# Performance work log

Measured on AMD Instinct MI355X. Metric: run time of the kernel, lower is better.

The kernel has to match this reference:

```python
import jax, jax.numpy as jnp
import numpy as np

HIDDEN = 4096
N_HEADS = 32
N_KV = 8
HEAD_DIM = HIDDEN // N_HEADS  # 128
ROT_DIM = int(HEAD_DIM * 0.5)  # partial_rotary_factor = 0.5 -> 64
ROPE_BASE = 1_000_000.0
EPS = 1e-6
T = 2048


def setup_inputs() -> dict:
    key = jax.random.key(0)
    k1, k2, k3, k4, k5 = jax.random.split(key, 5)
    qkv_out = (N_HEADS + 2 * N_KV) * HEAD_DIM  # 6144
    hidden_states = jax.random.normal(k1, (T, HIDDEN), dtype=jnp.float32)
    positions = jnp.arange(T, dtype=jnp.int32)
    w_qkv = jax.random.normal(k2, (HIDDEN, qkv_out), dtype=jnp.float32) * (HIDDEN ** -0.5)
    w_o = jax.random.normal(k3, (N_HEADS * HEAD_DIM, HIDDEN), dtype=jnp.float32) * ((N_HEADS * HEAD_DIM) ** -0.5)
    q_norm_w = jnp.ones((HEAD_DIM,), dtype=jnp.float32) + 0.01 * jax.random.normal(k4, (HEAD_DIM,), dtype=jnp.float32)
    k_norm_w = jnp.ones((HEAD_DIM,), dtype=jnp.float32) + 0.01 * jax.random.normal(k5, (HEAD_DIM,), dtype=jnp.float32)
    return {"hidden_states": hidden_states, "positions": positions,
            "w_qkv": w_qkv, "w_o": w_o, "q_norm_w": q_norm_w, "k_norm_w": k_norm_w}


def _rms_norm(x, w):
    # x: [T, H, D]; normalize over last dim
    var = jnp.mean(jnp.square(x), axis=-1, keepdims=True)
    return x * jax.lax.rsqrt(var + EPS) * w


def _apply_rope(x, positions):
    # neox-style rotary on first ROT_DIM dims of head_dim; rest passes through
    half = ROT_DIM // 2
    inv_freq = 1.0 / (ROPE_BASE ** (jnp.arange(0, ROT_DIM, 2, dtype=jnp.float32) / ROT_DIM))
    freqs = positions.astype(jnp.float32)[:, None] * inv_freq[None, :]  # [T, half]
    cos = jnp.cos(freqs)[:, None, :]  # [T, 1, half]
    sin = jnp.sin(freqs)[:, None, :]
    x_rot, x_pass = x[..., :ROT_DIM], x[..., ROT_DIM:]
    x1, x2 = x_rot[..., :half], x_rot[..., half:]
    rot = jnp.concatenate([x1 * cos - x2 * sin, x2 * cos + x1 * sin], axis=-1)
    return jnp.concatenate([rot, x_pass], axis=-1)


def reference(hidden_states, positions, w_qkv, w_o, q_norm_w, k_norm_w):
    q_size = N_HEADS * HEAD_DIM
    kv_size = N_KV * HEAD_DIM
    qkv = hidden_states @ w_qkv  # [T, q+2kv]
    q = qkv[:, :q_size].reshape(-1, N_HEADS, HEAD_DIM)
    k = qkv[:, q_size:q_size + kv_size].reshape(-1, N_KV, HEAD_DIM)
    v = qkv[:, q_size + kv_size:].reshape(-1, N_KV, HEAD_DIM)
    q = _rms_norm(q, q_norm_w)
    k = _rms_norm(k, k_norm_w)
    q = _apply_rope(q, positions)
    k = _apply_rope(k, positions)
    # GQA: repeat kv heads
    rep = N_HEADS // N_KV
    k = jnp.repeat(k, rep, axis=1)  # [T, H, D]
    v = jnp.repeat(v, rep, axis=1)
    scale = HEAD_DIM ** -0.5
    scores = jnp.einsum('thd,shd->hts', q, k) * scale  # [H, T, T]
    t = hidden_states.shape[0]
    causal = jnp.tril(jnp.ones((t, t), dtype=bool))
    scores = jnp.where(causal[None], scores, jnp.float32(-1e30))
    probs = jax.nn.softmax(scores, axis=-1)
    o = jnp.einsum('hts,shd->thd', probs, v).reshape(t, N_HEADS * HEAD_DIM)
    return o @ w_o
```

## Files before the change

kernel.cpp:

```cpp
#include <hip/hip_runtime.h>
#include <math.h>

#define HIDDEN 4096
#define QKV_N 6144
#define T_LEN 2048
#define HD 128
#define N_HEADS 32
#define N_KV 8
#define SCALE 0.08838834764831845f

typedef unsigned short u16;
typedef unsigned int u32;
typedef __attribute__((ext_vector_type(8))) short bf16x8;
typedef __attribute__((ext_vector_type(4))) float f32x4;

__device__ __forceinline__ u16 f2b(float x) {
  u32 u = __builtin_bit_cast(u32, x);
  u += 0x7fffu + ((u >> 16) & 1u);
  return (u16)(u >> 16);
}

typedef const __attribute__((address_space(1))) void* gas_ptr;
typedef __attribute__((address_space(3))) void* las_ptr;
__device__ __forceinline__ void gll16(const void* g, void* l) {
  __builtin_amdgcn_global_load_lds((gas_ptr)g, (las_ptr)l, 16, 0, 0);
}

__global__ __launch_bounds__(256) void cast_bf16_kernel(
    const float* __restrict__ in, u16* __restrict__ out) {
  const size_t i = ((size_t)blockIdx.x * 256 + threadIdx.x) * 4;
  f32x4 v = *(const f32x4*)(in + i);
  ushort4 o;
  o.x = f2b(v[0]); o.y = f2b(v[1]); o.z = f2b(v[2]); o.w = f2b(v[3]);
  *(ushort4*)(out + i) = o;
}

__global__ __launch_bounds__(256) void transpose_cast_kernel(
    const float* __restrict__ W, u16* __restrict__ WT, int K, int N) {
  __shared__ float t[32][33];
  const int n0 = blockIdx.x * 32, k0 = blockIdx.y * 32;
  const int c = threadIdx.x & 31;
  const int r0 = threadIdx.x >> 5;
#pragma unroll
  for (int j = 0; j < 4; ++j) {
    const int r = r0 + 8 * j;
    t[c][r] = W[(size_t)(k0 + r) * N + n0 + c];
  }
  __syncthreads();
#pragma unroll
  for (int j = 0; j < 4; ++j) {
    const int n = r0 + 8 * j;
    WT[(size_t)(n0 + n) * K + k0 + c] = f2b(t[n][c]);
  }
}

template <int BM, int BN, bool ROPE>
__global__ __launch_bounds__(512, 2) void gemm256_kernel(
    const u16* __restrict__ A, const u16* __restrict__ BT,
    float* __restrict__ C, int M, int N, int K,
    const int* __restrict__ positions, float2* __restrict__ ropeTab) {
  if constexpr (ROPE) {
    if (blockIdx.y == gridDim.y - 1) {
      for (int i = blockIdx.x * 512 + threadIdx.x; i < T_LEN * 32;
           i += gridDim.x * 512) {
        const int t = i >> 5, idx = i & 31;
        const float invf = powf(1.0e6f, -(float)idx * (1.0f / 32.0f));
        const float fr = (float)positions[t] * invf;
        ropeTab[i] = make_float2(cosf(fr), sinf(fr));
      }
      return;
    }
  }
  constexpr int WCOLS = BN / 4;
  constexpr int NF = WCOLS / 16;
  constexpr int NF2 = NF / 2;
  constexpr int MF = BM / 32;
  constexpr int ALOADS = BM / 128;
  constexpr int BLOADS = BN / 128;
  constexpr int VMN = ALOADS + BLOADS;
  __shared__ __align__(16) u16 As[2][2][BM * 32];
  __shared__ __align__(16) u16 Bs[2][2][BN * 32];

  const int tid = threadIdx.x;
  const int w = tid >> 6, l = tid & 63;
  const int wr = w >> 2, wc = w & 3;
  const int m = l & 15, g = l >> 4;
  const int bm = blockIdx.y * BM, bn = blockIdx.x * BN;
  const int NT = K >> 6;

  size_t gA[2]; int sA[2];
  size_t gB[2]; int sB[2];
#pragma unroll
  for (int i = 0; i < ALOADS; ++i) {
    const int s = i * 512 + tid;
    const int r = s >> 2, o = s & 3;
    sA[i] = s * 8;
    gA[i] = (size_t)(bm + r) * K + (o ^ ((r >> 1) & 3)) * 8;
  }
#pragma unroll
  for (int i = 0; i < BLOADS; ++i) {
    const int s = i * 512 + tid;
    const int r = s >> 2, o = s & 3;
    sB[i] = s * 8;
    gB[i] = (size_t)(bn + r) * K + (o ^ ((r >> 1) & 3)) * 8;
  }

  const int foff = m * 32 + ((g ^ ((m >> 1) & 3)) * 8);
  const int abase = wr * (BM / 2) * 32;
  const int bbase = wc * WCOLS * 32;

#define STAGE_A(tile, kh)                                                      \
  {                                                                            \
    const size_t kofs = (size_t)(tile) * 64 + (kh) * 32;                       \
    u16* dst = &As[(tile) & 1][kh][0];                                         \
    gll16(A + gA[0] + kofs, dst + sA[0]);                                      \
    if constexpr (ALOADS > 1) gll16(A + gA[1] + kofs, dst + sA[1]);            \
  }
#define STAGE_B(tile, kh)                                                      \
  {                                                                            \
    const size_t kofs = (size_t)(tile) * 64 + (kh) * 32;                       \
    u16* dst = &Bs[(tile) & 1][kh][0];                                         \
    gll16(BT + gB[0] + kofs, dst + sB[0]);                                     \
    if constexpr (BLOADS > 1) gll16(BT + gB[1] + kofs, dst + sB[1]);           \
  }
#define VM_COUNTED()                                                           \
  {                                                                            \
    if constexpr (VMN == 4)                                                    \
      asm volatile("s_waitcnt vmcnt(4)" ::: "memory");                         \
    else                                                                       \
      asm volatile("s_waitcnt vmcnt(3)" ::: "memory");                         \
  }
#define PHASE(j, b, DO_STAGE, tn, VM)                                          \
  {                                                                            \
    constexpr int qn = (j) & 1, kh = (j) >> 1;                                 \
    if constexpr (qn == 0) {                                                   \
      _Pragma("unroll") for (int fm = 0; fm < MF; ++fm)                        \
          af[fm] = *(const bf16x8*)(&As[b][kh][abase + fm * 512 + foff]);      \
    }                                                                          \
    bf16x8 bf[NF2];                                                            \
    _Pragma("unroll") for (int fn = 0; fn < NF2; ++fn)                         \
        bf[fn] =                                                               \
        *(const bf16x8*)(&Bs[b][kh][bbase + (qn * NF2 + fn) * 512 + foff]);    \
    if constexpr (DO_STAGE) {                                                  \
      if constexpr ((j) == 0) STAGE_A(tn, 0);                                  \
      if constexpr ((j) == 1) STAGE_B(tn, 0);                                  \
      if constexpr ((j) == 2) STAGE_A(tn, 1);                                  \
      if constexpr ((j) == 3) STAGE_B(tn, 1);                                  \
    }                                                                          \
    asm volatile("" ::: "memory");                                             \
    __builtin_amdgcn_s_barrier();                                              \
    asm volatile("" ::: "memory");                                             \
    __builtin_amdgcn_s_setprio(1);                                             \
    _Pragma("unroll") for (int fm = 0; fm < MF; ++fm)                          \
        _Pragma("unroll") for (int fn = 0; fn < NF2; ++fn)                     \
        acc[fm][qn * NF2 + fn] = __builtin_amdgcn_mfma_f32_16x16x32_bf16(      \
            af[fm], bf[fn], acc[fm][qn * NF2 + fn], 0, 0, 0);                  \
    __builtin_amdgcn_s_setprio(0);                                             \
    asm volatile("" ::: "memory");                                             \
    if constexpr (((j) & 1) && (VM) == 0)                                      \
      asm volatile("s_waitcnt vmcnt(0)" ::: "memory");                         \
    if constexpr (((j) & 1) && (VM) == 1) VM_COUNTED();                        \
    __builtin_amdgcn_s_barrier();                                              \
    asm volatile("" ::: "memory");                                             \
  }

  f32x4 acc[MF][NF];
#pragma unroll
  for (int i = 0; i < MF; ++i)
#pragma unroll
    for (int j = 0; j < NF; ++j) acc[i][j] = (f32x4){0.f, 0.f, 0.f, 0.f};

  STAGE_A(0, 0); STAGE_B(0, 0); STAGE_A(0, 1); STAGE_B(0, 1);
  VM_COUNTED();
  __builtin_amdgcn_s_barrier();
  asm volatile("" ::: "memory");

  bf16x8 af[MF];
  for (int t = 0; t < NT - 1; ++t) {
    const int b = t & 1, tn = t + 1;
    PHASE(0, b, true, tn, 1);
    PHASE(1, b, true, tn, 1);
    PHASE(2, b, true, tn, 1);
    PHASE(3, b, true, tn, 1);
  }
  {
    const int b = (NT - 1) & 1;
    PHASE(0, b, false, 0, 2);
    PHASE(1, b, false, 0, 0);
    PHASE(2, b, false, 0, 2);
    PHASE(3, b, false, 0, 2);
  }
#undef PHASE
#undef VM_COUNTED
#undef STAGE_B
#undef STAGE_A

#pragma unroll
  for (int fm = 0; fm < MF; ++fm) {
    const int row = bm + wr * (BM / 2) + fm * 16 + g * 4;
#pragma unroll
    for (int fn = 0; fn < NF; ++fn) {
      const int col = bn + wc * WCOLS + fn * 16 + m;
      float* cp = C + (size_t)row * N + col;
#pragma unroll
      for (int r = 0; r < 4; ++r) cp[(size_t)r * N] = acc[fm][fn][r];
    }
  }
}

__global__ __launch_bounds__(128) void normrope_pack_kernel(
    const float* __restrict__ qkv, const float2* __restrict__ tab,
    const float* __restrict__ qw, const float* __restrict__ kw,
    u16* __restrict__ Qp, u16* __restrict__ Kp) {
  const int t = blockIdx.x;
  const int hh = blockIdx.y;
  const int d = threadIdx.x;
  const bool isq = hh < N_HEADS;
  const int col = isq ? hh * HD : HIDDEN + (hh - N_HEADS) * HD;
  const float* row = qkv + (size_t)t * QKV_N + col;
  const float* w = isq ? qw : kw;

  float x = row[d];
  float ss = x * x;
#pragma unroll
  for (int off = 32; off >= 1; off >>= 1) ss += __shfl_xor(ss, off);
  __shared__ float wsum[2];
  __shared__ float xs[128];
  if ((d & 63) == 0) wsum[d >> 6] = ss;
  __syncthreads();
  const float tot = wsum[0] + wsum[1];
  const float inv = rsqrtf(tot * (1.f / 128.f) + 1e-6f);
  const float xn = x * inv * w[d];
  xs[d] = xn;
  __syncthreads();

  float outv;
  if (d < 64) {
    const int idx = d & 31;
    const float2 cs = tab[t * 32 + idx];
    const float x1 = xs[idx], x2 = xs[idx + 32];
    outv = (d < 32) ? (x1 * cs.x - x2 * cs.y) : (x2 * cs.x + x1 * cs.y);
  } else {
    outv = xn;
  }
  if (isq) {
    Qp[((size_t)hh * T_LEN + t) * HD + d] = f2b(outv * SCALE);
  } else {
    Kp[((size_t)(hh - N_HEADS) * T_LEN + t) * HD + d] = f2b(outv);
  }
}

__global__ __launch_bounds__(256) void vtrans_kernel(
    const float* __restrict__ qkv, u16* __restrict__ Vtp) {
  __shared__ float tile[32][132];
  const int t0 = blockIdx.x * 32;
  const int kvh = blockIdx.y;
  const int tv = threadIdx.x >> 3;
  const int c0 = (threadIdx.x & 7) * 16;
  const float* src =
      qkv + (size_t)(t0 + tv) * QKV_N + (HIDDEN + 1024) + kvh * HD + c0;
#pragma unroll
  for (int u = 0; u < 4; ++u)
    *(f32x4*)&tile[tv][c0 + 4 * u] = *(const f32x4*)(src + 4 * u);
  __syncthreads();
  const int dd = threadIdx.x >> 1;
  const int half = threadIdx.x & 1;
  u16 buf[16];
#pragma unroll
  for (int p = 0; p < 16; ++p) buf[p] = f2b(tile[half * 16 + p][dd]);
  u16* dst = Vtp + ((size_t)kvh * HD + dd) * T_LEN + t0 + half * 16;
  *(uint4*)dst = *(uint4*)&buf[0];
  *(uint4*)(dst + 8) = *(uint4*)&buf[8];
}

__global__ __launch_bounds__(256, 3) void attn4_kernel(
    const u16* __restrict__ Qp, const u16* __restrict__ Kp,
    const u16* __restrict__ Vtp, u16* __restrict__ outB,
    const float* __restrict__ w_o, u16* __restrict__ woT) {
  __shared__ __align__(16) u16 Qs[64 * 128];
  __shared__ __align__(16) u16 Ks[2 * 32 * 128];
  __shared__ __align__(16) u16 Vts[2 * 128 * 32];
  __shared__ __align__(16) u16 Plds[4 * 16 * 32];

  const int bx = blockIdx.x;
  const int h = blockIdx.y;
  const int tid = threadIdx.x;

  if (bx >= 16) {
    float(*tf)[33] = (float(*)[33])Qs;
    const int e = (bx - 16) + 8 * h;
    const int c = tid & 31, rr = tid >> 5;
    for (int tt = e * 64; tt < e * 64 + 64; ++tt) {
      const int n0 = (tt & 127) * 32, k0 = (tt >> 7) * 32;
#pragma unroll
      for (int j = 0; j < 4; ++j) {
        const int r = rr + 8 * j;
        tf[c][r] = w_o[(size_t)(k0 + r) * HIDDEN + n0 + c];
      }
      __syncthreads();
#pragma unroll
      for (int j = 0; j < 4; ++j) {
        const int n = rr + 8 * j;
        woT[(size_t)(n0 + n) * HIDDEN + k0 + c] = f2b(tf[n][c]);
      }
      __syncthreads();
    }
    return;
  }

  const int kvh = h >> 2;
  const int w = tid >> 6, l = tid & 63;
  const int g = l >> 4, m = l & 15;

  const u16* kbase = Kp + (size_t)kvh * T_LEN * HD;
  const u16* vbase = Vtp + (size_t)kvh * HD * T_LEN;
  u16* pl = Plds + w * 512;

#define STAGE_KV(jt, b)                                                        \
  {                                                                            \
    _Pragma("unroll") for (int p = 0; p < 2; ++p) {                            \
      const int krow = p * 16 + w * 4 + (l >> 4);                              \
      const int kg = (l & 15) ^ (krow & 7);                                    \
      gll16(kbase + (size_t)((jt) * 32 + krow) * 128 + kg * 8,                 \
            Ks + (b) * 4096 + p * 2048 + w * 512 + l * 8);                     \
      const int dv = p * 64 + w * 16 + (l >> 2);                               \
      const int vg = (l & 3) ^ ((dv >> 1) & 3);                                \
      gll16(vbase + (size_t)dv * T_LEN + (jt) * 32 + vg * 8,                   \
            Vts + (b) * 4096 + p * 2048 + w * 512 + l * 8);                    \
    }                                                                          \
  }

  for (int job = 0; job < 2; ++job) {
    const int qb = job ? bx : 31 - bx;
    const int t0 = qb * 64;
    const int NT = 2 * (qb + 1);

    {
      const u16* qbase = Qp + ((size_t)h * T_LEN + t0) * HD;
#pragma unroll
      for (int p = 0; p < 4; ++p) {
        const int row = p * 16 + w * 4 + (l >> 4);
        const int gr = (l & 15) ^ (row & 7);
        gll16(qbase + row * 128 + gr * 8, Qs + p * 2048 + w * 512 + l * 8);
      }
    }
    STAGE_KV(0, 0);
    __syncthreads();

    bf16x8 qf[4];
    {
      const u16* qr = Qs + (w * 16 + m) * 128;
#pragma unroll
      for (int kk = 0; kk < 4; ++kk)
        qf[kk] = *(const bf16x8*)(qr + (((kk * 4 + g) ^ (m & 7)) * 8));
    }

    f32x4 o[8];
#pragma unroll
    for (int n = 0; n < 8; ++n) o[n] = (f32x4){0.f, 0.f, 0.f, 0.f};
    float mrun = -1e30f, lrun = 0.f;

    for (int jt = 0; jt < NT; ++jt) {
      const int b = jt & 1;
      if (jt + 1 < NT) STAGE_KV(jt + 1, b ^ 1);

      f32x4 s[2];
      s[0] = (f32x4){0.f, 0.f, 0.f, 0.f};
      s[1] = (f32x4){0.f, 0.f, 0.f, 0.f};
      __builtin_amdgcn_s_setprio(1);
#pragma unroll
      for (int f = 0; f < 2; ++f) {
        const u16* kr = Ks + b * 4096 + (f * 16 + m) * 128;
#pragma unroll
        for (int kk = 0; kk < 4; ++kk) {
          bf16x8 kf = *(const bf16x8*)(kr + (((kk * 4 + g) ^ (m & 7)) * 8));
          s[f] =
              __builtin_amdgcn_mfma_f32_16x16x32_bf16(kf, qf[kk], s[f], 0, 0, 0);
        }
      }
      __builtin_amdgcn_s_setprio(0);

      if (jt >= NT - 2) {
        const int qg = t0 + w * 16 + m;
        const int kvb = jt * 32 + g * 4;
#pragma unroll
        for (int f = 0; f < 2; ++f)
#pragma unroll
          for (int r = 0; r < 4; ++r)
            if (kvb + f * 16 + r > qg) s[f][r] = -1e30f;
      }

      float pm = fmaxf(fmaxf(fmaxf(s[0][0], s[0][1]), fmaxf(s[0][2], s[0][3])),
                       fmaxf(fmaxf(s[1][0], s[1][1]), fmaxf(s[1][2], s[1][3])));
      pm = fmaxf(pm, __shfl_xor(pm, 16));
      pm = fmaxf(pm, __shfl_xor(pm, 32));
      if (!__all(pm <= mrun + 8.f)) {
        const float mn = fmaxf(mrun, pm);
        const float sc = __expf(mrun - mn);
        mrun = mn;
        lrun *= sc;
        f32x4 scr;
#pragma unroll
        for (int r = 0; r < 4; ++r) scr[r] = __shfl(sc, g * 4 + r);
#pragma unroll
        for (int n = 0; n < 8; ++n) o[n] *= scr;
      }
      float ps = 0.f;
#pragma unroll
      for (int f = 0; f < 2; ++f)
#pragma unroll
        for (int r = 0; r < 4; ++r) {
          s[f][r] = __expf(s[f][r] - mrun);
          ps += s[f][r];
        }
      ps += __shfl_xor(ps, 16);
      ps += __shfl_xor(ps, 32);
      lrun += ps;

      {
        const u32 a0 = (u32)f2b(s[0][0]) | ((u32)f2b(s[0][1]) << 16);
        const u32 a1 = (u32)f2b(s[0][2]) | ((u32)f2b(s[0][3]) << 16);
        const u32 b0 = (u32)f2b(s[1][0]) | ((u32)f2b(s[1][1]) << 16);
        const u32 b1 = (u32)f2b(s[1][2]) | ((u32)f2b(s[1][3]) << 16);
        *(uint2*)(pl + m * 32 + ((g ^ (m >> 1)) * 4)) = make_uint2(a0, a1);
        *(uint2*)(pl + m * 32 + (((g + 4) ^ (m >> 1)) * 4)) = make_uint2(b0, b1);
      }

      bf16x8 pa;
      {
        const uint2 lo =
            *(const uint2*)(pl + m * 32 + (((2 * g) ^ (m >> 1)) * 4));
        const uint2 hi =
            *(const uint2*)(pl + m * 32 + (((2 * g + 1) ^ (m >> 1)) * 4));
        union { u32 u[4]; bf16x8 v; } pu;
        pu.u[0] = lo.x; pu.u[1] = lo.y; pu.u[2] = hi.x; pu.u[3] = hi.y;
        pa = pu.v;
      }

      __builtin_amdgcn_s_setprio(1);
#pragma unroll
      for (int n = 0; n < 8; ++n) {
        const int dd = n * 16 + m;
        bf16x8 vf = *(const bf16x8*)(Vts + b * 4096 + dd * 32 +
                                     ((g ^ ((dd >> 1) & 3)) * 8));
        o[n] = __builtin_amdgcn_mfma_f32_16x16x32_bf16(pa, vf, o[n], 0, 0, 0);
      }
      __builtin_amdgcn_s_setprio(0);
      __syncthreads();
    }

    float li[4];
#pragma unroll
    for (int r = 0; r < 4; ++r) li[r] = 1.f / __shfl(lrun, g * 4 + r);
    u16* ob = outB + (size_t)(t0 + w * 16 + g * 4) * HIDDEN + h * HD + m;
#pragma unroll
    for (int n = 0; n < 8; ++n)
#pragma unroll
      for (int r = 0; r < 4; ++r)
        ob[(size_t)r * HIDDEN + n * 16] = f2b(o[n][r] * li[r]);
  }
#undef STAGE_KV
}

extern "C" void kernel_launch(void* const* d_in, const int* in_sizes, int n_in,
                              void* d_out, int out_size, void* d_ws,
                              size_t ws_size, hipStream_t stream) {
  const float* hidden = (const float*)d_in[0];
  const int* positions = (const int*)d_in[1];
  const float* w_qkv = (const float*)d_in[2];
  const float* w_o = (const float*)d_in[3];
  const float* q_norm_w = (const float*)d_in[4];
  const float* k_norm_w = (const float*)d_in[5];
  float* out = (float*)d_out;

  u16* hiddenB = (u16*)d_ws;
  u16* Qp = hiddenB;
  u16* wqkvT = hiddenB + (size_t)T_LEN * HIDDEN;
  u16* woT = wqkvT + (size_t)QKV_N * HIDDEN;
  float* qkv = (float*)(woT + (size_t)HIDDEN * HIDDEN);
  u16* attnB = (u16*)(qkv + (size_t)T_LEN * QKV_N);
  u16* Kp = attnB + (size_t)T_LEN * HIDDEN;
  u16* Vtp = Kp + (size_t)N_KV * T_LEN * HD;
  float2* ropeTab = (float2*)(Vtp + (size_t)N_KV * HD * T_LEN);

  cast_bf16_kernel<<<(T_LEN * HIDDEN) / 1024, 256, 0, stream>>>(hidden, hiddenB);
  transpose_cast_kernel<<<dim3(QKV_N / 32, HIDDEN / 32), 256, 0, stream>>>(
      w_qkv, wqkvT, HIDDEN, QKV_N);

  gemm256_kernel<256, 256, true>
      <<<dim3(QKV_N / 256, T_LEN / 256 + 1), 512, 0, stream>>>(
          hiddenB, wqkvT, qkv, T_LEN, QKV_N, HIDDEN, positions, ropeTab);
  normrope_pack_kernel<<<dim3(T_LEN, N_HEADS + N_KV), 128, 0, stream>>>(
      qkv, ropeTab, q_norm_w, k_norm_w, Qp, Kp);
  vtrans_kernel<<<dim3(T_LEN / 32, N_KV), 256, 0, stream>>>(qkv, Vtp);
  attn4_kernel<<<dim3(24, N_HEADS), 256, 0, stream>>>(Qp, Kp, Vtp, attnB, w_o,
                                                      woT);
  gemm256_kernel<128, 256, false>
      <<<dim3(HIDDEN / 256, T_LEN / 128), 512, 0, stream>>>(
          attnB, woT, out, T_LEN, HIDDEN, HIDDEN, nullptr, nullptr);
}
```

Before: 349.2 us.

## Fuse QK RMSNorm and RoPE into QKV GEMM epilogue

Result: slower. 363.1 us (+4.0%).

```diff
diff --git a/kernel.cpp b/kernel.cpp
--- a/kernel.cpp
+++ b/kernel.cpp
@@ -54,23 +54,12 @@
   }
 }
 
-template <int BM, int BN, bool ROPE>
+template <int BM, int BN, bool FUSE>
 __global__ __launch_bounds__(512, 2) void gemm256_kernel(
     const u16* __restrict__ A, const u16* __restrict__ BT,
     float* __restrict__ C, int M, int N, int K,
-    const int* __restrict__ positions, float2* __restrict__ ropeTab) {
-  if constexpr (ROPE) {
-    if (blockIdx.y == gridDim.y - 1) {
-      for (int i = blockIdx.x * 512 + threadIdx.x; i < T_LEN * 32;
-           i += gridDim.x * 512) {
-        const int t = i >> 5, idx = i & 31;
-        const float invf = powf(1.0e6f, -(float)idx * (1.0f / 32.0f));
-        const float fr = (float)positions[t] * invf;
-        ropeTab[i] = make_float2(cosf(fr), sinf(fr));
-      }
-      return;
-    }
-  }
+    const int* __restrict__ positions, const float* __restrict__ qw,
+    const float* __restrict__ kw, u16* __restrict__ Qp, u16* __restrict__ Kp) {
   constexpr int WCOLS = BN / 4;
   constexpr int NF = WCOLS / 16;
   constexpr int NF2 = NF / 2;
@@ -195,70 +184,111 @@
 #undef STAGE_B
 #undef STAGE_A
 
-#pragma unroll
-  for (int fm = 0; fm < MF; ++fm) {
-    const int row = bm + wr * (BM / 2) + fm * 16 + g * 4;
-#pragma unroll
-    for (int fn = 0; fn < NF; ++fn) {
-      const int col = bn + wc * WCOLS + fn * 16 + m;
-      float* cp = C + (size_t)row * N + col;
-#pragma unroll
-      for (int r = 0; r < 4; ++r) cp[(size_t)r * N] = acc[fm][fn][r];
+  if constexpr (FUSE) {
+    const int nb = blockIdx.x;
+    if (nb < 20) {
+      __syncthreads();
+      float* ssbuf = (float*)&As[0][0][0];
+      const bool isq = nb < 16;
+      const int dbase = (w & 1) * 64;
+      const int hsel = (w >> 1) & 1;
+      const float* wvec = isq ? qw : kw;
+      float wt[4];
+#pragma unroll
+      for (int fn = 0; fn < 4; ++fn) wt[fn] = wvec[dbase + fn * 16 + m];
+
+#pragma unroll
+      for (int fm = 0; fm < MF; ++fm)
+#pragma unroll
+        for (int r = 0; r < 4; ++r) {
+          float ss = 0.f;
+#pragma unroll
+          for (int fn = 0; fn < 4; ++fn) {
+            const float v = acc[fm][fn][r];
+            ss += v * v;
+          }
+          ss += __shfl_xor(ss, 1);
+          ss += __shfl_xor(ss, 2);
+          ss += __shfl_xor(ss, 4);
+          ss += __shfl_xor(ss, 8);
+          if (m == 0) ssbuf[w * 128 + fm * 16 + g * 4 + r] = ss;
+        }
+      __syncthreads();
+
+      const float invf0 = powf(1.0e6f, -(float)m * (1.0f / 32.0f));
+      const float invf1 = powf(1.0e6f, -(float)(16 + m) * (1.0f / 32.0f));
+      u16* outp = isq ? Qp + (size_t)(2 * nb + hsel) * T_LEN * HD
+                      : Kp + (size_t)(2 * (nb - 16) + hsel) * T_LEN * HD;
+      const float oscale = isq ? SCALE : 1.0f;
+
+#pragma unroll
+      for (int fm = 0; fm < MF; ++fm) {
+#pragma unroll
+        for (int r = 0; r < 4; ++r) {
+          const int lrow = fm * 16 + g * 4 + r;
+          const int t = bm + wr * 128 + lrow;
+          const float tot = ssbuf[w * 128 + lrow] + ssbuf[(w ^ 1) * 128 + lrow];
+          const float inv = rsqrtf(tot * (1.0f / 128.0f) + 1e-6f);
+          float xn[4];
+#pragma unroll
+          for (int fn = 0; fn < 4; ++fn) xn[fn] = acc[fm][fn][r] * inv * wt[fn];
+          float o0, o1, o2, o3;
+          if ((w & 1) == 0) {
+            const float p = (float)positions[t];
+            const float fr0 = p * invf0, fr1 = p * invf1;
+            const float c0 = cosf(fr0), s0 = sinf(fr0);
+            const float c1 = cosf(fr1), s1 = sinf(fr1);
+            o0 = xn[0] * c0 - xn[2] * s0;
+            o1 = xn[1] * c1 - xn[3] * s1;
+            o2 = xn[2] * c0 + xn[0] * s0;
+            o3 = xn[3] * c1 + xn[1] * s1;
+          } else {
+            o0 = xn[0]; o1 = xn[1]; o2 = xn[2]; o3 = xn[3];
+          }
+          u16* op = outp + (size_t)t * HD + dbase + m;
+          op[0] = f2b(o0 * oscale);
+          op[16] = f2b(o1 * oscale);
+          op[32] = f2b(o2 * oscale);
+          op[48] = f2b(o3 * oscale);
+        }
+      }
+    } else {
+      const int vb = (nb - 20) * 256;
+#pragma unroll
+      for (int fm = 0; fm < MF; ++fm) {
+        const int row = bm + wr * 128 + fm * 16 + g * 4;
+#pragma unroll
+        for (int fn = 0; fn < NF; ++fn) {
+          const int col = vb + wc * WCOLS + fn * 16 + m;
+          float* cp = C + (size_t)row * 1024 + col;
+#pragma unroll
+          for (int r = 0; r < 4; ++r) cp[(size_t)r * 1024] = acc[fm][fn][r];
+        }
+      }
     }
-  }
-}
-
-__global__ __launch_bounds__(128) void normrope_pack_kernel(
-    const float* __restrict__ qkv, const float2* __restrict__ tab,
-    const float* __restrict__ qw, const float* __restrict__ kw,
-    u16* __restrict__ Qp, u16* __restrict__ Kp) {
-  const int t = blockIdx.x;
-  const int hh = blockIdx.y;
-  const int d = threadIdx.x;
-  const bool isq = hh < N_HEADS;
-  const int col = isq ? hh * HD : HIDDEN + (hh - N_HEADS) * HD;
-  const float* row = qkv + (size_t)t * QKV_N + col;
-  const float* w = isq ? qw : kw;
-
-  float x = row[d];
-  float ss = x * x;
-#pragma unroll
-  for (int off = 32; off >= 1; off >>= 1) ss += __shfl_xor(ss, off);
-  __shared__ float wsum[2];
-  __shared__ float xs[128];
-  if ((d & 63) == 0) wsum[d >> 6] = ss;
-  __syncthreads();
-  const float tot = wsum[0] + wsum[1];
-  const float inv = rsqrtf(tot * (1.f / 128.f) + 1e-6f);
-  const float xn = x * inv * w[d];
-  xs[d] = xn;
-  __syncthreads();
-
-  float outv;
-  if (d < 64) {
-    const int idx = d & 31;
-    const float2 cs = tab[t * 32 + idx];
-    const float x1 = xs[idx], x2 = xs[idx + 32];
-    outv = (d < 32) ? (x1 * cs.x - x2 * cs.y) : (x2 * cs.x + x1 * cs.y);
   } else {
-    outv = xn;
-  }
-  if (isq) {
-    Qp[((size_t)hh * T_LEN + t) * HD + d] = f2b(outv * SCALE);
-  } else {
-    Kp[((size_t)(hh - N_HEADS) * T_LEN + t) * HD + d] = f2b(outv);
+#pragma unroll
+    for (int fm = 0; fm < MF; ++fm) {
+      const int row = bm + wr * (BM / 2) + fm * 16 + g * 4;
+#pragma unroll
+      for (int fn = 0; fn < NF; ++fn) {
+        const int col = bn + wc * WCOLS + fn * 16 + m;
+        float* cp = C + (size_t)row * N + col;
+#pragma unroll
+        for (int r = 0; r < 4; ++r) cp[(size_t)r * N] = acc[fm][fn][r];
+      }
+    }
   }
 }
 
 __global__ __launch_bounds__(256) void vtrans_kernel(
-    const float* __restrict__ qkv, u16* __restrict__ Vtp) {
+    const float* __restrict__ Vf32, u16* __restrict__ Vtp) {
   __shared__ float tile[32][132];
   const int t0 = blockIdx.x * 32;
   const int kvh = blockIdx.y;
   const int tv = threadIdx.x >> 3;
   const int c0 = (threadIdx.x & 7) * 16;
-  const float* src =
-      qkv + (size_t)(t0 + tv) * QKV_N + (HIDDEN + 1024) + kvh * HD + c0;
+  const float* src = Vf32 + (size_t)(t0 + tv) * 1024 + kvh * HD + c0;
 #pragma unroll
   for (int u = 0; u < 4; ++u)
     *(f32x4*)&tile[tv][c0 + 4 * u] = *(const f32x4*)(src + 4 * u);
@@ -474,28 +504,27 @@
   float* out = (float*)d_out;
 
   u16* hiddenB = (u16*)d_ws;
-  u16* Qp = hiddenB;
   u16* wqkvT = hiddenB + (size_t)T_LEN * HIDDEN;
   u16* woT = wqkvT + (size_t)QKV_N * HIDDEN;
-  float* qkv = (float*)(woT + (size_t)HIDDEN * HIDDEN);
-  u16* attnB = (u16*)(qkv + (size_t)T_LEN * QKV_N);
+  float* Vf32 = (float*)(woT + (size_t)HIDDEN * HIDDEN);
+  u16* attnB = (u16*)(Vf32 + (size_t)T_LEN * 1024);
   u16* Kp = attnB + (size_t)T_LEN * HIDDEN;
   u16* Vtp = Kp + (size_t)N_KV * T_LEN * HD;
-  float2* ropeTab = (float2*)(Vtp + (size_t)N_KV * HD * T_LEN);
+  u16* Qp = Vtp + (size_t)N_KV * HD * T_LEN;
 
   cast_bf16_kernel<<<(T_LEN * HIDDEN) / 1024, 256, 0, stream>>>(hidden, hiddenB);
   transpose_cast_kernel<<<dim3(QKV_N / 32, HIDDEN / 32), 256, 0, stream>>>(
       w_qkv, wqkvT, HIDDEN, QKV_N);
 
   gemm256_kernel<256, 256, true>
-      <<<dim3(QKV_N / 256, T_LEN / 256 + 1), 512, 0, stream>>>(
-          hiddenB, wqkvT, qkv, T_LEN, QKV_N, HIDDEN, positions, ropeTab);
-  normrope_pack_kernel<<<dim3(T_LEN, N_HEADS + N_KV), 128, 0, stream>>>(
-      qkv, ropeTab, q_norm_w, k_norm_w, Qp, Kp);
-  vtrans_kernel<<<dim3(T_LEN / 32, N_KV), 256, 0, stream>>>(qkv, Vtp);
+      <<<dim3(QKV_N / 256, T_LEN / 256), 512, 0, stream>>>(
+          hiddenB, wqkvT, Vf32, T_LEN, 1024, HIDDEN, positions, q_norm_w,
+          k_norm_w, Qp, Kp);
+  vtrans_kernel<<<dim3(T_LEN / 32, N_KV), 256, 0, stream>>>(Vf32, Vtp);
   attn4_kernel<<<dim3(24, N_HEADS), 256, 0, stream>>>(Qp, Kp, Vtp, attnB, w_o,
                                                       woT);
   gemm256_kernel<128, 256, false>
       <<<dim3(HIDDEN / 256, T_LEN / 128), 512, 0, stream>>>(
-          attnB, woT, out, T_LEN, HIDDEN, HIDDEN, nullptr, nullptr);
-}
+          attnB, woT, out, T_LEN, HIDDEN, HIDDEN, nullptr, nullptr, nullptr,
+          nullptr, nullptr);
+}
```
